# Optimization experiments

Measured on AMD Instinct MI355X. Metric: run time of the kernel, lower is better.

## Reference

```python
import jax, jax.numpy as jnp
import numpy as np

SEQ, BATCH, FEATURES, D_MODEL, N_LAYER = 2048, 64, 64, 256, 2


def setup_inputs() -> dict:
    key = jax.random.key(0)
    ks = jax.random.split(key, 10)
    s = 0.05
    H = D_MODEL
    return {
        "input_ids": jax.random.normal(ks[0], (SEQ, BATCH, FEATURES), jnp.float32),
        "enc_w": jax.random.normal(ks[1], (H, FEATURES), jnp.float32) * s,
        "enc_b": jax.random.normal(ks[2], (H,), jnp.float32) * s,
        # PyTorch LSTM layout: gates stacked as [i, f, g, o] along first axis
        "w_ih": jax.random.normal(ks[3], (N_LAYER, 4 * H, H), jnp.float32) * s,
        "w_hh": jax.random.normal(ks[4], (N_LAYER, 4 * H, H), jnp.float32) * s,
        "b_ih": jax.random.normal(ks[5], (N_LAYER, 4 * H), jnp.float32) * s,
        "b_hh": jax.random.normal(ks[6], (N_LAYER, 4 * H), jnp.float32) * s,
        "dec_w": jax.random.normal(ks[7], (FEATURES, H), jnp.float32) * s,
        "dec_b": jax.random.normal(ks[8], (FEATURES,), jnp.float32) * s,
    }


def _lstm_layer(x, w_ih_l, w_hh_l, b_ih_l, b_hh_l):
    # x: (S, B, H). Precompute input projections for all timesteps at once.
    S, B, H = x.shape
    xg = jnp.einsum('sbh,gh->sbg', x, w_ih_l) + b_ih_l + b_hh_l  # (S, B, 4H)

    def step(carry, xg_t):
        h, c = carry
        gates = xg_t + h @ w_hh_l.T  # (B, 4H)
        i, f, g, o = jnp.split(gates, 4, axis=-1)
        i = jax.nn.sigmoid(i)
        f = jax.nn.sigmoid(f)
        g = jnp.tanh(g)
        o = jax.nn.sigmoid(o)
        c = f * c + i * g
        h = o * jnp.tanh(c)
        return (h, c), h

    h0 = jnp.zeros((B, H), x.dtype)
    c0 = jnp.zeros((B, H), x.dtype)
    _, ys = jax.lax.scan(step, (h0, c0), xg)
    return ys  # (S, B, H)


def reference(input_ids, enc_w, enc_b, w_ih, w_hh, b_ih, b_hh, dec_w, dec_b):
    x = input_ids @ enc_w.T + enc_b  # (S, B, H)
    n_layer = w_ih.shape[0]
    for l in range(n_layer):
        x = _lstm_layer(x, w_ih[l], w_hh[l], b_ih[l], b_hh[l])
    return x @ dec_w.T + dec_b  # (S, B, features)
```

## Files before the change

kernel.cpp:

```cpp
#include <hip/hip_runtime.h>


typedef unsigned short u16;
typedef unsigned long long u64;
typedef __attribute__((ext_vector_type(8))) short short8;
typedef __attribute__((ext_vector_type(4))) float f32x4;

#define SEQ  2048
#define CS   128
#define NCH  (SEQ / CS)
#define CN   (CS * 64)
#define SLOT 16384
#define HXBYTES ((size_t)(CS + 1) * SLOT * 2)
#define SENT64 0x7F7F7F7F7F7F7F7FULL

__device__ __forceinline__ u16 f2bf(float f) {
  unsigned u = __float_as_uint(f);
  unsigned r = u + 0x7fffu + ((u >> 16) & 1u);
  return (u16)(r >> 16);
}
__device__ __forceinline__ float bf2f(u16 h) {
  return __uint_as_float(((unsigned)h) << 16);
}
__device__ __forceinline__ float sigf(float x) {
  return __builtin_amdgcn_rcpf(1.f + __expf(-x));
}
__device__ __forceinline__ float tanhf_fast(float x) {
  return 1.f - 2.f * __builtin_amdgcn_rcpf(1.f + __expf(2.f * x));
}

__device__ __forceinline__ u64 aload(const u16* p) {
  return __hip_atomic_load((const u64*)p, __ATOMIC_RELAXED, __HIP_MEMORY_SCOPE_AGENT);
}
__device__ __forceinline__ void astore(u16* p, u64 v) {
  __hip_atomic_store((u64*)p, v, __ATOMIC_RELAXED, __HIP_MEMORY_SCOPE_AGENT);
}

__device__ __forceinline__ void ld8_issue(const u16* a0, u64 v[8]) {
  asm volatile(
      "global_load_dwordx2 %0, %8, off sc0 sc1\n\t"
      "global_load_dwordx2 %1, %8, off offset:2048 sc0 sc1\n\t"
      "global_load_dwordx2 %2, %9, off sc0 sc1\n\t"
      "global_load_dwordx2 %3, %9, off offset:2048 sc0 sc1\n\t"
      "global_load_dwordx2 %4, %10, off sc0 sc1\n\t"
      "global_load_dwordx2 %5, %10, off offset:2048 sc0 sc1\n\t"
      "global_load_dwordx2 %6, %11, off sc0 sc1\n\t"
      "global_load_dwordx2 %7, %11, off offset:2048 sc0 sc1"
      : "=&v"(v[0]), "=&v"(v[1]), "=&v"(v[2]), "=&v"(v[3]),
        "=&v"(v[4]), "=&v"(v[5]), "=&v"(v[6]), "=&v"(v[7])
      : "v"(a0), "v"(a0 + 2048), "v"(a0 + 4096), "v"(a0 + 6144)
      : "memory");
}
__device__ __forceinline__ void vmwait8(u64 v[8]) {
  asm volatile("s_waitcnt vmcnt(0)"
      : "+v"(v[0]), "+v"(v[1]), "+v"(v[2]), "+v"(v[3]),
        "+v"(v[4]), "+v"(v[5]), "+v"(v[6]), "+v"(v[7]) :: "memory");
}
__device__ __forceinline__ void ld8_agent(const u16* a0, u64 v[8]) {
  ld8_issue(a0, v);
  vmwait8(v);
}

__device__ __forceinline__ void wg_barrier() {
  __builtin_amdgcn_sched_barrier(0);
  asm volatile("s_waitcnt lgkmcnt(0)" ::: "memory");
  __builtin_amdgcn_s_barrier();
  __builtin_amdgcn_sched_barrier(0);
}

__device__ __forceinline__ int rowp_to_orig(int rowp) {
  int p = rowp >> 8, T = (rowp >> 4) & 15, u = rowp & 15;
  int g = u & 3;
  int j = ((T >> 2) << 4) + ((u >> 2) << 2) + (T & 3);
  return g * 256 + p * 64 + j;
}

#define PREP_TOTAL (16384 + 65536 + 1024 + 1024 + 524288 + 262144 + 32768)

__global__ void prep_kernel(const float* __restrict__ enc_w, const float* __restrict__ enc_b,
                            const float* __restrict__ w_ih, const float* __restrict__ w_hh,
                            const float* __restrict__ b_ih, const float* __restrict__ b_hh,
                            const float* __restrict__ dec_w,
                            u16* __restrict__ WDEC, u16* __restrict__ CW,
                            float* __restrict__ CB, float* __restrict__ B1P,
                            u16* __restrict__ WHHP, u16* __restrict__ WIH1P,
                            u16* __restrict__ HX0, u16* __restrict__ HX1)
{
  size_t idx = (size_t)blockIdx.x * 256 + threadIdx.x;
  if (idx < 16384) { WDEC[idx] = f2bf(dec_w[idx]); return; }
  idx -= 16384;
  if (idx < 65536) {
    int rowp = (int)(idx >> 6), f = (int)(idx & 63);
    int r = rowp_to_orig(rowp);
    float a = 0.f;
    for (int k = 0; k < 256; ++k) a += w_ih[r * 256 + k] * enc_w[k * 64 + f];
    CW[idx] = f2bf(a);
    return;
  }
  idx -= 65536;
  if (idx < 1024) {
    int r = rowp_to_orig((int)idx);
    float a = b_ih[r] + b_hh[r];
    for (int k = 0; k < 256; ++k) a += w_ih[r * 256 + k] * enc_b[k];
    CB[idx] = a;
    return;
  }
  idx -= 1024;
  if (idx < 1024) {
    int r = rowp_to_orig((int)idx);
    B1P[idx] = b_ih[1024 + r] + b_hh[1024 + r];
    return;
  }
  idx -= 1024;
  if (idx < 524288) {
    int l = (int)(idx >> 18);
    int rem = (int)(idx & 262143);
    int e = rem & 7, lane = (rem >> 3) & 63, kc = (rem >> 9) & 7;
    int t = (rem >> 12) & 3, wv = (rem >> 14) & 3, pp = (rem >> 16) & 3;
    int u = lane & 15, qd = lane >> 4;
    int g = u & 3;
    int j = wv * 16 + ((u >> 2) << 2) + t;
    int r = g * 256 + pp * 64 + j;
    int k = kc * 32 + qd * 8 + e;
    WHHP[idx] = f2bf(w_hh[(size_t)l * 262144 + (size_t)r * 256 + k]);
    return;
  }
  idx -= 524288;
  if (idx < 262144) {
    int rem = (int)idx;
    int e = rem & 7, lane = (rem >> 3) & 63, kc = (rem >> 9) & 7;
    int t = (rem >> 12) & 3, wv = (rem >> 14) & 3, pp = (rem >> 16) & 3;
    int u = lane & 15, qd = lane >> 4;
    int g = u & 3;
    int j = wv * 16 + ((u >> 2) << 2) + t;
    int r = g * 256 + pp * 64 + j;
    int k = kc * 32 + qd * 8 + e;
    WIH1P[idx] = f2bf(w_ih[262144 + (size_t)r * 256 + k]);
    return;
  }
  idx -= 262144;
  if (idx < 32768) {
    if (idx < 16384) HX0[idx] = 0;
    else             HX1[idx - 16384] = 0;
  }
}

template<int KTILES, int OUTBF, int BMODE, int AF32>
__global__ __launch_bounds__(256, 1) void gemm_bt(
    const void* __restrict__ Av, const u16* __restrict__ B, void* __restrict__ Cv,
    const float* __restrict__ bias, size_t ldc)
{
  constexpr int K = KTILES * 64;
  __shared__ __align__(16) u16 Asl[64 * 72];
  __shared__ __align__(16) u16 Bsl[64 * 72];
  const int tid = threadIdx.x;
  const int w = tid >> 6, lane = tid & 63, lm = lane & 15, quad = lane >> 4;
  const size_t m0 = (size_t)blockIdx.y * 64, n0 = (size_t)blockIdx.x * 64;

  f32x4 acc[4];
#pragma unroll
  for (int nt = 0; nt < 4; ++nt) { f32x4 z = {0.f, 0.f, 0.f, 0.f}; acc[nt] = z; }

  for (int kb = 0; kb < KTILES; ++kb) {
    if (AF32) {
      const float* Af = (const float*)Av;
#pragma unroll
      for (int c = 0; c < 4; ++c) {
        int idx = c * 256 + tid;
        int row = idx >> 4, k4 = idx & 15;
        float4 v = *(const float4*)(Af + (m0 + row) * (size_t)K + kb * 64 + k4 * 4);
        u64 pv = (u64)f2bf(v.x) | ((u64)f2bf(v.y) << 16) |
                 ((u64)f2bf(v.z) << 32) | ((u64)f2bf(v.w) << 48);
        *(u64*)(&Asl[row * 72 + k4 * 4]) = pv;
      }
    } else {
      const u16* Ab = (const u16*)Av;
#pragma unroll
      for (int c = 0; c < 2; ++c) {
        int idx = c * 256 + tid;
        int row = idx >> 3, k8 = idx & 7;
        *(uint4*)(&Asl[row * 72 + k8 * 8]) =
            *(const uint4*)(Ab + (m0 + row) * (size_t)K + kb * 64 + k8 * 8);
      }
    }
#pragma unroll
    for (int c = 0; c < 2; ++c) {
      int idx = c * 256 + tid;
      int row = idx >> 3, k8 = idx & 7;
      *(uint4*)(&Bsl[row * 72 + k8 * 8]) =
          *(const uint4*)(B + (n0 + row) * (size_t)K + kb * 64 + k8 * 8);
    }
    __syncthreads();
#pragma unroll
    for (int kc = 0; kc < 2; ++kc) {
      short8 a = *(const short8*)(&Asl[(w * 16 + lm) * 72 + kc * 32 + quad * 8]);
#pragma unroll
      for (int nt = 0; nt < 4; ++nt) {
        short8 b = *(const short8*)(&Bsl[(nt * 16 + lm) * 72 + kc * 32 + quad * 8]);
        acc[nt] = __builtin_amdgcn_mfma_f32_16x16x32_bf16(a, b, acc[nt], 0, 0, 0);
      }
    }
    __syncthreads();
  }
#pragma unroll
  for (int nt = 0; nt < 4; ++nt) {
    size_t n = n0 + nt * 16 + lm;
    float bn = (BMODE == 1) ? bias[n] : 0.f;
#pragma unroll
    for (int r = 0; r < 4; ++r) {
      size_t m = m0 + w * 16 + quad * 4 + r;
      float v = acc[nt][r] + ((BMODE == 2) ? bias[m] : bn);
      if (OUTBF) ((u16*)Cv)[m * ldc + n] = f2bf(v);
      else       ((float*)Cv)[m * ldc + n] = v;
    }
  }
}

__device__ __forceinline__ void gather32(const u16* __restrict__ src,
                                         u16* __restrict__ dst,
                                         int tid, int n2, bool skip, int p)
{
  const int j4 = tid & 63;
  const int tw = tid >> 6;
  const bool need = !(skip && ((j4 >> 4) == p));
  if (!need) return;
  const u16* a0 = src + ((size_t)(n2 * 32 + tw) * 256 + j4 * 4);
  u64 v[8];
  ld8_agent(a0, v);
  for (;;) {
    bool bad = false;
#pragma unroll
    for (int i = 0; i < 8; ++i) bad |= (v[i] == SENT64);
    if (!bad) break;
    ld8_agent(a0, v);
  }
#pragma unroll
  for (int i = 0; i < 8; ++i)
    *(u64*)(dst + (i * 4 + tw) * 264 + j4 * 4) = v[i];
}

__global__ __launch_bounds__(256, 1) void lstm_fused(
    const u16* __restrict__ xg0, u16* __restrict__ x2,
    const u16* __restrict__ whhp, const u16* __restrict__ wih1p,
    const float* __restrict__ b1p,
    u16* __restrict__ hx0, u16* __restrict__ hx1,
    float* __restrict__ cstb, int base)
{
  __shared__ __align__(16) u16 Hl[2][2][32 * 264];
  const int tid = threadIdx.x;
  const int role = blockIdx.x;
  const int layer = role >> 3, p = role & 3, n2 = (role >> 2) & 1;
  const int lane = tid & 63, w = tid >> 6, lm = lane & 15, quad = lane >> 4;
  const int j4 = tid & 63, tw = tid >> 6;

  short8 wfh[4][8], wfi[4][8];
  {
    const u16* wp = whhp + (size_t)((layer * 4 + p) * 4 + w) * 16384 + lane * 8;
#pragma unroll
    for (int t = 0; t < 4; ++t)
#pragma unroll
      for (int kc = 0; kc < 8; ++kc)
        wfh[t][kc] = *(const short8*)(wp + (t * 8 + kc) * 512);
  }
  f32x4 bias_f[4];
  if (layer) {
    const u16* wp = wih1p + (size_t)(p * 4 + w) * 16384 + lane * 8;
#pragma unroll
    for (int t = 0; t < 4; ++t)
#pragma unroll
      for (int kc = 0; kc < 8; ++kc)
        wfi[t][kc] = *(const short8*)(wp + (t * 8 + kc) * 512);
#pragma unroll
    for (int t = 0; t < 4; ++t)
      bias_f[t] = *(const f32x4*)(b1p + p * 256 + (w * 4 + t) * 16 + quad * 4);
  }

  float* cp = cstb + (size_t)(((layer * 4 + p) * 2 + n2) * 256 + tid) * 8;
  float cst[4][2];
  if (base) {
#pragma unroll
    for (int t = 0; t < 4; ++t) { cst[t][0] = cp[t * 2]; cst[t][1] = cp[t * 2 + 1]; }
  } else {
#pragma unroll
    for (int t = 0; t < 4; ++t) { cst[t][0] = 0.f; cst[t][1] = 0.f; }
  }

  const int jcol = p * 64 + w * 16 + quad * 4;
  u16* myhx = layer ? hx1 : hx0;
  u64 hprev[2] = {0, 0};

  for (int s = 1; s <= CS; ++s) {
    const int cur = s & 1;
    const bool own = (s > 1);
    f32x4 acc[4][2];

    if (layer == 0) {
      u64 xv[4][2];
#pragma unroll
      for (int t = 0; t < 4; ++t)
#pragma unroll
        for (int nt = 0; nt < 2; ++nt)
          xv[t][nt] = *(const u64*)(xg0 +
              ((size_t)(s - 1) * 64 + n2 * 32 + nt * 16 + lm) * 1024 +
              p * 256 + (w * 4 + t) * 16 + quad * 4);
      gather32(hx0 + (size_t)(s - 1) * SLOT, &Hl[cur][0][0], tid, n2, own, p);
      if (own) {
#pragma unroll
        for (int nt = 0; nt < 2; ++nt)
          *(u64*)(&Hl[cur][0][(nt * 16 + lm) * 264 + jcol]) = hprev[nt];
      }
      wg_barrier();
#pragma unroll
      for (int t = 0; t < 4; ++t)
#pragma unroll
        for (int nt = 0; nt < 2; ++nt) {
          u64 v = xv[t][nt];
          f32x4 tt = { bf2f((u16)v), bf2f((u16)(v >> 16)),
                       bf2f((u16)(v >> 32)), bf2f((u16)(v >> 48)) };
          acc[t][nt] = tt;
        }
#pragma unroll
      for (int kc = 0; kc < 8; ++kc) {
        short8 b0[2];
#pragma unroll
        for (int nt = 0; nt < 2; ++nt)
          b0[nt] = *(const short8*)(&Hl[cur][0][(nt * 16 + lm) * 264 + kc * 32 + quad * 8]);
#pragma unroll
        for (int t = 0; t < 4; ++t)
#pragma unroll
          for (int nt = 0; nt < 2; ++nt)
            acc[t][nt] = __builtin_amdgcn_mfma_f32_16x16x32_bf16(
                wfh[t][kc], b0[nt], acc[t][nt], 0, 0, 0);
      }
    } else {
      gather32(hx1 + (size_t)(s - 1) * SLOT, &Hl[cur][1][0], tid, n2, own, p);
      if (own) {
#pragma unroll
        for (int nt = 0; nt < 2; ++nt)
          *(u64*)(&Hl[cur][1][(nt * 16 + lm) * 264 + jcol]) = hprev[nt];
      }
      const u16* ah = hx0 + (size_t)s * SLOT +
                      ((size_t)(n2 * 32 + tw) * 256 + j4 * 4);
      u64 vh[8];
      ld8_issue(ah, vh);
      wg_barrier();
#pragma unroll
      for (int t = 0; t < 4; ++t)
#pragma unroll
        for (int nt = 0; nt < 2; ++nt) acc[t][nt] = bias_f[t];
#pragma unroll
      for (int kc = 0; kc < 8; ++kc) {
        short8 b1[2];
#pragma unroll
        for (int nt = 0; nt < 2; ++nt)
          b1[nt] = *(const short8*)(&Hl[cur][1][(nt * 16 + lm) * 264 + kc * 32 + quad * 8]);
#pragma unroll
        for (int t = 0; t < 4; ++t)
#pragma unroll
          for (int nt = 0; nt < 2; ++nt)
            acc[t][nt] = __builtin_amdgcn_mfma_f32_16x16x32_bf16(
                wfh[t][kc], b1[nt], acc[t][nt], 0, 0, 0);
      }
      vmwait8(vh);
      for (;;) {
        bool bad = false;
#pragma unroll
        for (int i = 0; i < 8; ++i) bad |= (vh[i] == SENT64);
        if (!bad) break;
        ld8_agent(ah, vh);
      }
#pragma unroll
      for (int i = 0; i < 8; ++i)
        *(u64*)(&Hl[cur][0][(i * 4 + tw) * 264 + j4 * 4]) = vh[i];
      wg_barrier();
#pragma unroll
      for (int kc = 0; kc < 8; ++kc) {
        short8 b0[2];
#pragma unroll
        for (int nt = 0; nt < 2; ++nt)
          b0[nt] = *(const short8*)(&Hl[cur][0][(nt * 16 + lm) * 264 + kc * 32 + quad * 8]);
#pragma unroll
        for (int t = 0; t < 4; ++t)
#pragma unroll
          for (int nt = 0; nt < 2; ++nt)
            acc[t][nt] = __builtin_amdgcn_mfma_f32_16x16x32_bf16(
                wfi[t][kc], b0[nt], acc[t][nt], 0, 0, 0);
      }
    }

    u16* hd = myhx + (size_t)s * SLOT;
#pragma unroll
    for (int nt = 0; nt < 2; ++nt) {
      u64 h = 0;
#pragma unroll
      for (int t = 0; t < 4; ++t) {
        float iv = sigf(acc[t][nt][0]);
        float fv = sigf(acc[t][nt][1]);
        float gv = tanhf_fast(acc[t][nt][2]);
        float ov = sigf(acc[t][nt][3]);
        float cv = fv * cst[t][nt] + iv * gv;
        cst[t][nt] = cv;
        h |= (u64)f2bf(ov * tanhf_fast(cv)) << (16 * t);
      }
      const int b = n2 * 32 + nt * 16 + lm;
      astore(hd + (size_t)b * 256 + jcol, h);
      if (s == CS) astore(myhx + (size_t)b * 256 + jcol, h);
      if (layer) *(u64*)(x2 + ((size_t)(s - 1) * 64 + b) * 256 + jcol) = h;
      hprev[nt] = h;
    }
  }
#pragma unroll
  for (int t = 0; t < 4; ++t) { cp[t * 2] = cst[t][0]; cp[t * 2 + 1] = cst[t][1]; }
}

extern "C" void kernel_launch(void* const* d_in, const int* in_sizes, int n_in,
                              void* d_out, int out_size, void* d_ws, size_t ws_size,
                              hipStream_t stream)
{
  const float* in0   = (const float*)d_in[0];
  const float* enc_w = (const float*)d_in[1];
  const float* enc_b = (const float*)d_in[2];
  const float* w_ih  = (const float*)d_in[3];
  const float* w_hh  = (const float*)d_in[4];
  const float* b_ih  = (const float*)d_in[5];
  const float* b_hh  = (const float*)d_in[6];
  const float* dec_w = (const float*)d_in[7];
  const float* dec_b = (const float*)d_in[8];

  char* ws = (char*)d_ws;
  u16*   XG    = (u16*)(ws);
  u16*   X2    = (u16*)(ws + 16777216);
  u16*   WHHP  = (u16*)(ws + 20971520);
  u16*   WIH1P = (u16*)(ws + 22020096);
  u16*   CW    = (u16*)(ws + 22544384);
  u16*   WDEC  = (u16*)(ws + 22675456);
  float* CB    = (float*)(ws + 22708224);
  float* B1P   = (float*)(ws + 22712320);
  u16*   HX0   = (u16*)(ws + 22716416);
  u16*   HX1   = (u16*)(ws + 26943488);
  float* CST   = (float*)(ws + 31170560);

  if (ws_size < 31301632) return;

  hipMemsetAsync(HX0, 0x7F, HXBYTES, stream);
  hipMemsetAsync(HX1, 0x7F, HXBYTES, stream);

  prep_kernel<<<dim3((PREP_TOTAL + 255) / 256), 256, 0, stream>>>(
      enc_w, enc_b, w_ih, w_hh, b_ih, b_hh, dec_w,
      WDEC, CW, CB, B1P, WHHP, WIH1P, HX0, HX1);

  for (int c = 0; c < NCH; ++c) {
    const float* inc = in0 + (size_t)c * CN * 64;
    float* outc = (float*)d_out + (size_t)c * CN * 64;
    gemm_bt<1, 1, 1, 1><<<dim3(16, CN / 64), 256, 0, stream>>>(inc, CW, XG, CB, 1024);
    lstm_fused<<<dim3(16), 256, 0, stream>>>(XG, X2, WHHP, WIH1P, B1P,
                                             HX0, HX1, CST, c * CS);
    if (c + 1 < NCH) {
      hipMemsetAsync((char*)HX0 + SLOT * 2, 0x7F, HXBYTES - SLOT * 2, stream);
      hipMemsetAsync((char*)HX1 + SLOT * 2, 0x7F, HXBYTES - SLOT * 2, stream);
    }
    gemm_bt<4, 0, 1, 0><<<dim3(1, CN / 64), 256, 0, stream>>>(X2, WDEC, (void*)outc, dec_b, 64);
  }

  (void)in_sizes; (void)n_in; (void)out_size;
}
```

Measured before the change: 7.554 ms.

## Place LSTM role groups by XCC to use L2-coherent polling loads

Launches 32 blocks for the 16 roles. Each block reads its XCC id from a hardware register, and the blocks rendezvous through a global counter. Blocks are then ranked so that cooperating role groups land on the same XCC, and the spare blocks exit. When a group shares an XCC, the h-state polling uses sc0-only loads, which can hit the shared L2, instead of loads that bypass the cache. Stores write twice, a plain store plus an atomic store, to keep both paths visible. The change also prefetches the next timestep's layer-0 input projections one step ahead and adds a layer-1 path that gathers h0 into LDS. In exchange it adds a spin-wait rendezvous on every launch and relies on the blocks being co-resident, on undocumented XCC placement, and on cache-coherence assumptions.

```diff
diff --git a/kernel.cpp b/kernel.cpp
--- a/kernel.cpp
+++ b/kernel.cpp
@@ -34,6 +34,9 @@
 }
 __device__ __forceinline__ void astore(u16* p, u64 v) {
   __hip_atomic_store((u64*)p, v, __ATOMIC_RELAXED, __HIP_MEMORY_SCOPE_AGENT);
+}
+__device__ __forceinline__ void st_plain(u16* p, u64 v) {
+  asm volatile("global_store_dwordx2 %0, %1, off" :: "v"(p), "v"(v));
 }
 
 __device__ __forceinline__ void ld8_issue(const u16* a0, u64 v[8]) {
@@ -60,6 +63,22 @@
   ld8_issue(a0, v);
   vmwait8(v);
 }
+__device__ __forceinline__ void ld8_sc0(const u16* a0, u64 v[8]) {
+  asm volatile(
+      "global_load_dwordx2 %0, %8, off sc0\n\t"
+      "global_load_dwordx2 %1, %8, off offset:2048 sc0\n\t"
+      "global_load_dwordx2 %2, %9, off sc0\n\t"
+      "global_load_dwordx2 %3, %9, off offset:2048 sc0\n\t"
+      "global_load_dwordx2 %4, %10, off sc0\n\t"
+      "global_load_dwordx2 %5, %10, off offset:2048 sc0\n\t"
+      "global_load_dwordx2 %6, %11, off sc0\n\t"
+      "global_load_dwordx2 %7, %11, off offset:2048 sc0\n\t"
+      "s_waitcnt vmcnt(0)"
+      : "=&v"(v[0]), "=&v"(v[1]), "=&v"(v[2]), "=&v"(v[3]),
+        "=&v"(v[4]), "=&v"(v[5]), "=&v"(v[6]), "=&v"(v[7])
+      : "v"(a0), "v"(a0 + 2048), "v"(a0 + 4096), "v"(a0 + 6144)
+      : "memory");
+}
 
 __device__ __forceinline__ void wg_barrier() {
   __builtin_amdgcn_sched_barrier(0);
@@ -75,7 +94,7 @@
   return g * 256 + p * 64 + j;
 }
 
-#define PREP_TOTAL (16384 + 65536 + 1024 + 1024 + 524288 + 262144 + 32768)
+#define PREP_TOTAL (16384 + 65536 + 1024 + 1024 + 524288 + 262144 + 32768 + 64)
 
 __global__ void prep_kernel(const float* __restrict__ enc_w, const float* __restrict__ enc_b,
                             const float* __restrict__ w_ih, const float* __restrict__ w_hh,
@@ -84,7 +103,8 @@
                             u16* __restrict__ WDEC, u16* __restrict__ CW,
                             float* __restrict__ CB, float* __restrict__ B1P,
                             u16* __restrict__ WHHP, u16* __restrict__ WIH1P,
-                            u16* __restrict__ HX0, u16* __restrict__ HX1)
+                            u16* __restrict__ HX0, u16* __restrict__ HX1,
+                            int* __restrict__ RDV)
 {
   size_t idx = (size_t)blockIdx.x * 256 + threadIdx.x;
   if (idx < 16384) { WDEC[idx] = f2bf(dec_w[idx]); return; }
@@ -142,7 +162,10 @@
   if (idx < 32768) {
     if (idx < 16384) HX0[idx] = 0;
     else             HX1[idx - 16384] = 0;
-  }
+    return;
+  }
+  idx -= 32768;
+  if (idx < 64) RDV[idx] = 0;
 }
 
 template<int KTILES, int OUTBF, int BMODE, int AF32>
@@ -218,21 +241,21 @@
 
 __device__ __forceinline__ void gather32(const u16* __restrict__ src,
                                          u16* __restrict__ dst,
-                                         int tid, int n2, bool skip, int p)
+                                         int tid, int n2, bool skip, int p,
+                                         bool fastmode)
 {
   const int j4 = tid & 63;
   const int tw = tid >> 6;
-  const bool need = !(skip && ((j4 >> 4) == p));
-  if (!need) return;
+  if (skip && ((j4 >> 4) == p)) return;
   const u16* a0 = src + ((size_t)(n2 * 32 + tw) * 256 + j4 * 4);
   u64 v[8];
-  ld8_agent(a0, v);
-  for (;;) {
+  if (fastmode) ld8_sc0(a0, v); else ld8_agent(a0, v);
+  for (int r = 1;; ++r) {
     bool bad = false;
 #pragma unroll
     for (int i = 0; i < 8; ++i) bad |= (v[i] == SENT64);
     if (!bad) break;
-    ld8_agent(a0, v);
+    if (fastmode && (r & 3)) ld8_sc0(a0, v); else ld8_agent(a0, v);
   }
 #pragma unroll
   for (int i = 0; i < 8; ++i)
@@ -244,12 +267,53 @@
     const u16* __restrict__ whhp, const u16* __restrict__ wih1p,
     const float* __restrict__ b1p,
     u16* __restrict__ hx0, u16* __restrict__ hx1,
-    float* __restrict__ cstb, int base)
+    float* __restrict__ cstb, int* __restrict__ RDV, int base)
 {
   __shared__ __align__(16) u16 Hl[2][2][32 * 264];
+  __shared__ int sh_role, sh_pf, sh_h0f;
   const int tid = threadIdx.x;
-  const int role = blockIdx.x;
-  const int layer = role >> 3, p = role & 3, n2 = (role >> 2) & 1;
+  const int bid = blockIdx.x;
+
+  {
+    int myxcc = __builtin_amdgcn_s_getreg(6164) & 7;
+    if (tid == 0) {
+      __hip_atomic_store(&RDV[bid], myxcc, __ATOMIC_RELAXED, __HIP_MEMORY_SCOPE_AGENT);
+      __hip_atomic_fetch_add(&RDV[32], 1, __ATOMIC_RELEASE, __HIP_MEMORY_SCOPE_AGENT);
+      const int tgt = 32 * (base / CS + 1);
+      while (__hip_atomic_load(&RDV[32], __ATOMIC_ACQUIRE, __HIP_MEMORY_SCOPE_AGENT) < tgt) {}
+    }
+    __syncthreads();
+    if (tid < 64) {
+      int id  = (tid < 32) ? (__hip_atomic_load(&RDV[tid], __ATOMIC_RELAXED,
+                                                __HIP_MEMORY_SCOPE_AGENT) & 7) : 7;
+      int key = (tid < 32) ? ((id << 8) | tid) : 0x7FFFFFFF;
+      int rank = 0;
+#pragma unroll
+      for (int j = 0; j < 32; ++j) {
+        int kj = __shfl(key, j);
+        rank += (kj < key) ? 1 : 0;
+      }
+      int myrank = __shfl(rank, bid);
+      int myid   = __shfl(id, bid);
+      int g  = myrank >> 2;
+      int sg = (myrank >> 3) << 1;
+      u64 bg  = __ballot(tid < 32 && (rank >> 2) == g);
+      u64 bgm = __ballot(tid < 32 && (rank >> 2) == g  && id == myid);
+      u64 bs  = __ballot(tid < 32 && (rank >> 2) == sg);
+      u64 bsm = __ballot(tid < 32 && (rank >> 2) == sg && id == myid);
+      if (tid == 0) {
+        sh_role = (myrank < 16) ? myrank : -1;
+        sh_pf   = (bg == bgm) ? 1 : 0;
+        sh_h0f  = (bs == bsm) ? 1 : 0;
+      }
+    }
+    __syncthreads();
+  }
+  const int role = sh_role;
+  if (role < 0) return;
+  const bool fast   = sh_pf != 0;
+  const bool h0fast = sh_h0f != 0;
+  const int p = role & 3, layer = (role >> 2) & 1, n2 = role >> 3;
   const int lane = tid & 63, w = tid >> 6, lm = lane & 15, quad = lane >> 4;
   const int j4 = tid & 63, tw = tid >> 6;
 
@@ -288,6 +352,17 @@
   const int jcol = p * 64 + w * 16 + quad * 4;
   u16* myhx = layer ? hx1 : hx0;
   u64 hprev[2] = {0, 0};
+
+  u64 xva[4][2], xvb[4][2];
+  if (layer == 0) {
+#pragma unroll
+    for (int t = 0; t < 4; ++t)
+#pragma unroll
+      for (int nt = 0; nt < 2; ++nt)
+        xva[t][nt] = *(const u64*)(xg0 +
+            ((size_t)0 * 64 + n2 * 32 + nt * 16 + lm) * 1024 +
+            p * 256 + (w * 4 + t) * 16 + quad * 4);
+  }
 
   for (int s = 1; s <= CS; ++s) {
     const int cur = s & 1;
@@ -295,26 +370,27 @@
     f32x4 acc[4][2];
 
     if (layer == 0) {
-      u64 xv[4][2];
+      gather32(hx0 + (size_t)(s - 1) * SLOT, &Hl[cur][0][0], tid, n2, own, p, fast);
+      if (own) {
+#pragma unroll
+        for (int nt = 0; nt < 2; ++nt)
+          *(u64*)(&Hl[cur][0][(nt * 16 + lm) * 264 + jcol]) = hprev[nt];
+      }
+      if (s < CS) {
+#pragma unroll
+        for (int t = 0; t < 4; ++t)
+#pragma unroll
+          for (int nt = 0; nt < 2; ++nt)
+            xvb[t][nt] = *(const u64*)(xg0 +
+                ((size_t)s * 64 + n2 * 32 + nt * 16 + lm) * 1024 +
+                p * 256 + (w * 4 + t) * 16 + quad * 4);
+      }
+      wg_barrier();
 #pragma unroll
       for (int t = 0; t < 4; ++t)
 #pragma unroll
-        for (int nt = 0; nt < 2; ++nt)
-          xv[t][nt] = *(const u64*)(xg0 +
-              ((size_t)(s - 1) * 64 + n2 * 32 + nt * 16 + lm) * 1024 +
-              p * 256 + (w * 4 + t) * 16 + quad * 4);
-      gather32(hx0 + (size_t)(s - 1) * SLOT, &Hl[cur][0][0], tid, n2, own, p);
-      if (own) {
-#pragma unroll
-        for (int nt = 0; nt < 2; ++nt)
-          *(u64*)(&Hl[cur][0][(nt * 16 + lm) * 264 + jcol]) = hprev[nt];
-      }
-      wg_barrier();
-#pragma unroll
-      for (int t = 0; t < 4; ++t)
-#pragma unroll
         for (int nt = 0; nt < 2; ++nt) {
-          u64 v = xv[t][nt];
+          u64 v = xva[t][nt];
           f32x4 tt = { bf2f((u16)v), bf2f((u16)(v >> 16)),
                        bf2f((u16)(v >> 32)), bf2f((u16)(v >> 48)) };
           acc[t][nt] = tt;
@@ -332,8 +408,47 @@
             acc[t][nt] = __builtin_amdgcn_mfma_f32_16x16x32_bf16(
                 wfh[t][kc], b0[nt], acc[t][nt], 0, 0, 0);
       }
+    } else if (h0fast) {
+      gather32(hx1 + (size_t)(s - 1) * SLOT, &Hl[cur][1][0], tid, n2, own, p, fast);
+      if (own) {
+#pragma unroll
+        for (int nt = 0; nt < 2; ++nt)
+          *(u64*)(&Hl[cur][1][(nt * 16 + lm) * 264 + jcol]) = hprev[nt];
+      }
+      gather32(hx0 + (size_t)s * SLOT, &Hl[cur][0][0], tid, n2, false, p, true);
+      wg_barrier();
+#pragma unroll
+      for (int t = 0; t < 4; ++t)
+#pragma unroll
+        for (int nt = 0; nt < 2; ++nt) acc[t][nt] = bias_f[t];
+#pragma unroll
+      for (int kc = 0; kc < 8; ++kc) {
+        short8 b0[2];
+#pragma unroll
+        for (int nt = 0; nt < 2; ++nt)
+          b0[nt] = *(const short8*)(&Hl[cur][0][(nt * 16 + lm) * 264 + kc * 32 + quad * 8]);
+#pragma unroll
+        for (int t = 0; t < 4; ++t)
+#pragma unroll
+          for (int nt = 0; nt < 2; ++nt)
+            acc[t][nt] = __builtin_amdgcn_mfma_f32_16x16x32_bf16(
+                wfi[t][kc], b0[nt], acc[t][nt], 0, 0, 0);
+      }
+#pragma unroll
+      for (int kc = 0; kc < 8; ++kc) {
+        short8 b1[2];
+#pragma unroll
+        for (int nt = 0; nt < 2; ++nt)
+          b1[nt] = *(const short8*)(&Hl[cur][1][(nt * 16 + lm) * 264 + kc * 32 + quad * 8]);
+#pragma unroll
+        for (int t = 0; t < 4; ++t)
+#pragma unroll
+          for (int nt = 0; nt < 2; ++nt)
+            acc[t][nt] = __builtin_amdgcn_mfma_f32_16x16x32_bf16(
+                wfh[t][kc], b1[nt], acc[t][nt], 0, 0, 0);
+      }
     } else {
-      gather32(hx1 + (size_t)(s - 1) * SLOT, &Hl[cur][1][0], tid, n2, own, p);
+      gather32(hx1 + (size_t)(s - 1) * SLOT, &Hl[cur][1][0], tid, n2, own, p, fast);
       if (own) {
 #pragma unroll
         for (int nt = 0; nt < 2; ++nt)
@@ -403,10 +518,22 @@
         h |= (u64)f2bf(ov * tanhf_fast(cv)) << (16 * t);
       }
       const int b = n2 * 32 + nt * 16 + lm;
-      astore(hd + (size_t)b * 256 + jcol, h);
-      if (s == CS) astore(myhx + (size_t)b * 256 + jcol, h);
+      u16* pd = hd + (size_t)b * 256 + jcol;
+      st_plain(pd, h);
+      astore(pd, h);
+      if (s == CS) {
+        u16* ps = myhx + (size_t)b * 256 + jcol;
+        st_plain(ps, h);
+        astore(ps, h);
+      }
       if (layer) *(u64*)(x2 + ((size_t)(s - 1) * 64 + b) * 256 + jcol) = h;
       hprev[nt] = h;
+    }
+    if (layer == 0 && s < CS) {
+#pragma unroll
+      for (int t = 0; t < 4; ++t)
+#pragma unroll
+        for (int nt = 0; nt < 2; ++nt) xva[t][nt] = xvb[t][nt];
     }
   }
 #pragma unroll
@@ -439,22 +566,23 @@
   u16*   HX0   = (u16*)(ws + 22716416);
   u16*   HX1   = (u16*)(ws + 26943488);
   float* CST   = (float*)(ws + 31170560);
-
-  if (ws_size < 31301632) return;
+  int*   RDV   = (int*)(ws + 31301632);
+
+  if (ws_size < 31301888) return;
 
   hipMemsetAsync(HX0, 0x7F, HXBYTES, stream);
   hipMemsetAsync(HX1, 0x7F, HXBYTES, stream);
 
   prep_kernel<<<dim3((PREP_TOTAL + 255) / 256), 256, 0, stream>>>(
       enc_w, enc_b, w_ih, w_hh, b_ih, b_hh, dec_w,
-      WDEC, CW, CB, B1P, WHHP, WIH1P, HX0, HX1);
+      WDEC, CW, CB, B1P, WHHP, WIH1P, HX0, HX1, RDV);
 
   for (int c = 0; c < NCH; ++c) {
     const float* inc = in0 + (size_t)c * CN * 64;
     float* outc = (float*)d_out + (size_t)c * CN * 64;
     gemm_bt<1, 1, 1, 1><<<dim3(16, CN / 64), 256, 0, stream>>>(inc, CW, XG, CB, 1024);
-    lstm_fused<<<dim3(16), 256, 0, stream>>>(XG, X2, WHHP, WIH1P, B1P,
-                                             HX0, HX1, CST, c * CS);
+    lstm_fused<<<dim3(32), 256, 0, stream>>>(XG, X2, WHHP, WIH1P, B1P,
+                                             HX0, HX1, CST, RDV, c * CS);
     if (c + 1 < NCH) {
       hipMemsetAsync((char*)HX0 + SLOT * 2, 0x7F, HXBYTES - SLOT * 2, stream);
       hipMemsetAsync((char*)HX1 + SLOT * 2, 0x7F, HXBYTES - SLOT * 2, stream);
```

New measurement: 12.26 ms. 62.3% more time.

## Load layer-0 hidden-state MFMA fragments directly from global, skipping LDS staging

Applied to the files above, without the earlier changes.

For layer 0, each lane now polls the previous step's h directly from global memory in MFMA B-fragment layout (16 dwordx4 loads with sentinel check), instead of gathering into LDS, inserting its own hprev, and barrier-syncing. This removes the LDS write/read round trip and the workgroup barrier from the recurrent critical path. In exchange, each wave redundantly loads the full h slice, including its own-produced part, which adds global traffic. The wait is also on the slowest slice, and a retry reloads all 16 vectors.

```diff
diff --git a/kernel.cpp b/kernel.cpp
--- a/kernel.cpp
+++ b/kernel.cpp
@@ -5,6 +5,7 @@
 typedef unsigned long long u64;
 typedef __attribute__((ext_vector_type(8))) short short8;
 typedef __attribute__((ext_vector_type(4))) float f32x4;
+typedef __attribute__((ext_vector_type(4))) unsigned int u32x4;
 
 #define SEQ  2048
 #define CS   128
@@ -13,6 +14,7 @@
 #define SLOT 16384
 #define HXBYTES ((size_t)(CS + 1) * SLOT * 2)
 #define SENT64 0x7F7F7F7F7F7F7F7FULL
+#define S32    0x7F7F7F7Fu
 
 __device__ __forceinline__ u16 f2bf(float f) {
   unsigned u = __float_as_uint(f);
@@ -29,9 +31,6 @@
   return 1.f - 2.f * __builtin_amdgcn_rcpf(1.f + __expf(2.f * x));
 }
 
-__device__ __forceinline__ u64 aload(const u16* p) {
-  return __hip_atomic_load((const u64*)p, __ATOMIC_RELAXED, __HIP_MEMORY_SCOPE_AGENT);
-}
 __device__ __forceinline__ void astore(u16* p, u64 v) {
   __hip_atomic_store((u64*)p, v, __ATOMIC_RELAXED, __HIP_MEMORY_SCOPE_AGENT);
 }
@@ -59,6 +58,43 @@
 __device__ __forceinline__ void ld8_agent(const u16* a0, u64 v[8]) {
   ld8_issue(a0, v);
   vmwait8(v);
+}
+
+__device__ __forceinline__ void ldf16_drain(const u16* a0, const u16* a1, u32x4 f[16]) {
+  asm volatile(
+      "global_load_dwordx4 %0, %16, off sc0 sc1\n\t"
+      "global_load_dwordx4 %1, %16, off offset:64 sc0 sc1\n\t"
+      "global_load_dwordx4 %2, %16, off offset:128 sc0 sc1\n\t"
+      "global_load_dwordx4 %3, %16, off offset:192 sc0 sc1\n\t"
+      "global_load_dwordx4 %4, %16, off offset:256 sc0 sc1\n\t"
+      "global_load_dwordx4 %5, %16, off offset:320 sc0 sc1\n\t"
+      "global_load_dwordx4 %6, %16, off offset:384 sc0 sc1\n\t"
+      "global_load_dwordx4 %7, %16, off offset:448 sc0 sc1\n\t"
+      "global_load_dwordx4 %8, %17, off sc0 sc1\n\t"
+      "global_load_dwordx4 %9, %17, off offset:64 sc0 sc1\n\t"
+      "global_load_dwordx4 %10, %17, off offset:128 sc0 sc1\n\t"
+      "global_load_dwordx4 %11, %17, off offset:192 sc0 sc1\n\t"
+      "global_load_dwordx4 %12, %17, off offset:256 sc0 sc1\n\t"
+      "global_load_dwordx4 %13, %17, off offset:320 sc0 sc1\n\t"
+      "global_load_dwordx4 %14, %17, off offset:384 sc0 sc1\n\t"
+      "global_load_dwordx4 %15, %17, off offset:448 sc0 sc1\n\t"
+      "s_waitcnt vmcnt(0)"
+      : "=&v"(f[0]),  "=&v"(f[1]),  "=&v"(f[2]),  "=&v"(f[3]),
+        "=&v"(f[4]),  "=&v"(f[5]),  "=&v"(f[6]),  "=&v"(f[7]),
+        "=&v"(f[8]),  "=&v"(f[9]),  "=&v"(f[10]), "=&v"(f[11]),
+        "=&v"(f[12]), "=&v"(f[13]), "=&v"(f[14]), "=&v"(f[15])
+      : "v"(a0), "v"(a1)
+      : "memory");
+}
+__device__ __forceinline__ void pollf16_drain(const u16* a0, const u16* a1, u32x4 f[16]) {
+  for (;;) {
+    ldf16_drain(a0, a1, f);
+    unsigned bad = 0;
+#pragma unroll
+    for (int i = 0; i < 16; ++i)
+      bad |= (f[i].x == S32) | (f[i].y == S32) | (f[i].z == S32) | (f[i].w == S32);
+    if (!bad) return;
+  }
 }
 
 __device__ __forceinline__ void wg_barrier() {
@@ -222,8 +258,7 @@
 {
   const int j4 = tid & 63;
   const int tw = tid >> 6;
-  const bool need = !(skip && ((j4 >> 4) == p));
-  if (!need) return;
+  if (skip && ((j4 >> 4) == p)) return;
   const u16* a0 = src + ((size_t)(n2 * 32 + tw) * 256 + j4 * 4);
   u64 v[8];
   ld8_agent(a0, v);
@@ -288,6 +323,7 @@
   const int jcol = p * 64 + w * 16 + quad * 4;
   u16* myhx = layer ? hx1 : hx0;
   u64 hprev[2] = {0, 0};
+  const size_t fro = ((size_t)(n2 * 32 + lm) * 256 + quad * 8);
 
   for (int s = 1; s <= CS; ++s) {
     const int cur = s & 1;
@@ -303,13 +339,10 @@
           xv[t][nt] = *(const u64*)(xg0 +
               ((size_t)(s - 1) * 64 + n2 * 32 + nt * 16 + lm) * 1024 +
               p * 256 + (w * 4 + t) * 16 + quad * 4);
-      gather32(hx0 + (size_t)(s - 1) * SLOT, &Hl[cur][0][0], tid, n2, own, p);
-      if (own) {
-#pragma unroll
-        for (int nt = 0; nt < 2; ++nt)
-          *(u64*)(&Hl[cur][0][(nt * 16 + lm) * 264 + jcol]) = hprev[nt];
-      }
-      wg_barrier();
+      const u16* fb0 = hx0 + (size_t)(s - 1) * SLOT + fro;
+      const u16* fb1 = fb0 + 16 * 256;
+      u32x4 fr[16];
+      pollf16_drain(fb0, fb1, fr);
 #pragma unroll
       for (int t = 0; t < 4; ++t)
 #pragma unroll
@@ -321,16 +354,13 @@
         }
 #pragma unroll
       for (int kc = 0; kc < 8; ++kc) {
-        short8 b0[2];
-#pragma unroll
-        for (int nt = 0; nt < 2; ++nt)
-          b0[nt] = *(const short8*)(&Hl[cur][0][(nt * 16 + lm) * 264 + kc * 32 + quad * 8]);
-#pragma unroll
-        for (int t = 0; t < 4; ++t)
-#pragma unroll
-          for (int nt = 0; nt < 2; ++nt)
-            acc[t][nt] = __builtin_amdgcn_mfma_f32_16x16x32_bf16(
-                wfh[t][kc], b0[nt], acc[t][nt], 0, 0, 0);
+        short8 b0 = __builtin_bit_cast(short8, fr[kc]);
+        short8 b1 = __builtin_bit_cast(short8, fr[8 + kc]);
+#pragma unroll
+        for (int t = 0; t < 4; ++t) {
+          acc[t][0] = __builtin_amdgcn_mfma_f32_16x16x32_bf16(wfh[t][kc], b0, acc[t][0], 0, 0, 0);
+          acc[t][1] = __builtin_amdgcn_mfma_f32_16x16x32_bf16(wfh[t][kc], b1, acc[t][1], 0, 0, 0);
+        }
       }
     } else {
       gather32(hx1 + (size_t)(s - 1) * SLOT, &Hl[cur][1][0], tid, n2, own, p);
```

After: 11.30 ms. 49.6% more time.
